# Performance work log

Hardware: AMD Instinct MI355X
Metric: run time of the kernel (lower is better)

Reference implementation:

```python
import jax, jax.numpy as jnp
import numpy as np

INPUT_DIM = 8
HIDDEN_DIM = 128
MID = 50
T = 4096
# original: tsteps = linspace(t0, t1, int(2 + (t1-t0)//0.1)); with t1-t0 == 1.0,
# 1.0//0.1 == 9.0 in float arithmetic -> 11 points -> 10 uniform Euler substeps.
K_SUB = 10


def setup_inputs() -> dict:
    key = jax.random.key(0)
    ks = jax.random.split(key, 12)
    x = jax.random.normal(ks[0], (T, INPUT_DIM), dtype=jnp.float32)
    # arange pairs (2i, 2i+1): every interval has t1 - t0 == 1.0
    dt = jnp.arange(T * 2, dtype=jnp.float32).reshape(T, 2)
    s = 0.1  # init.normal_(std=0.1) in LODEFunc; reuse for heads
    W1 = jax.random.normal(ks[1], (INPUT_DIM + HIDDEN_DIM, MID), dtype=jnp.float32) * s
    b1 = jnp.zeros((MID,), dtype=jnp.float32)
    W2 = jax.random.normal(ks[2], (MID, HIDDEN_DIM), dtype=jnp.float32) * s
    b2 = jnp.zeros((HIDDEN_DIM,), dtype=jnp.float32)
    Wls1 = jax.random.normal(ks[3], (HIDDEN_DIM, HIDDEN_DIM), dtype=jnp.float32) * s
    bls1 = jax.random.normal(ks[4], (HIDDEN_DIM,), dtype=jnp.float32) * s
    wls2 = jax.random.normal(ks[5], (HIDDEN_DIM,), dtype=jnp.float32) * s
    bls2 = jax.random.normal(ks[6], (), dtype=jnp.float32) * s
    Wlm1 = jax.random.normal(ks[7], (HIDDEN_DIM, HIDDEN_DIM), dtype=jnp.float32) * s
    blm1 = jax.random.normal(ks[8], (HIDDEN_DIM,), dtype=jnp.float32) * s
    return {"x": x, "dt": dt, "W1": W1, "b1": b1, "W2": W2, "b2": b2,
            "Wls1": Wls1, "bls1": bls1, "wls2": wls2, "bls2": bls2,
            "Wlm1": Wlm1, "blm1": blm1}


def reference(x, dt, W1, b1, W2, b2, Wls1, bls1, wls2, bls2, Wlm1, blm1):
    def ode_func(z, xi):
        # LODEFunc: tanh(Linear(tanh(Linear(cat(z, x)))))
        zx = jnp.concatenate([z, xi])  # [H + I]
        h1 = jnp.tanh(zx @ W1 + b1)    # [50]
        return jnp.tanh(h1 @ W2 + b2)  # [H]

    def step(z, inp):
        xi, dti = inp
        hstep = (dti[1] - dti[0]) / K_SUB  # uniform Euler step (0 interval -> no-op)
        z = jax.lax.fori_loop(0, K_SUB, lambda j, zz: zz + hstep * ode_func(zz, xi), z)
        pre_sigma = jnp.tanh(z @ Wls1 + bls1)
        sigma = jax.nn.softplus(pre_sigma @ wls2 + bls2)
        pre_mu = jnp.tanh(z @ Wlm1 + blm1)
        mu = pre_mu @ wls2 + bls2  # NOTE: original reuses self.ls2 for mu (faithful)
        return z, (mu, sigma)

    z0 = jnp.zeros((HIDDEN_DIM,), dtype=x.dtype)
    _, (mu_out, sigma_out) = jax.lax.scan(step, z0, (x, dt))
    return mu_out[:, None], sigma_out[:, None]  # each [T, 1]
```

## Files before the change

### kernel.cpp

```cpp
#include <hip/hip_runtime.h>
#include <hip/hip_bf16.h>

#define T_STEPS 4096
#define HID 128
#define INP 8
#define MID 50
#define KSUB 10

typedef float v2f __attribute__((ext_vector_type(2)));

__device__ __forceinline__ v2f mk2(float a, float b){ v2f r; r.x = a; r.y = b; return r; }
__device__ __forceinline__ v2f bc2(float s){ v2f r; r.x = s; r.y = s; return r; }

__device__ __forceinline__ v2f fma2(v2f a, v2f b, v2f c){
#if __has_builtin(__builtin_elementwise_fma)
    return __builtin_elementwise_fma(a, b, c);
#else
    c.x = fmaf(a.x, b.x, c.x); c.y = fmaf(a.y, b.y, c.y); return c;
#endif
}

__device__ __forceinline__ float rlane(float v, int i){
    return __int_as_float(__builtin_amdgcn_readlane(__float_as_int(v), i));
}

__device__ __forceinline__ float fast_tanh(float x){
    float e = __expf(2.0f * x);
    return 1.0f - 2.0f / (e + 1.0f);
}
__device__ __forceinline__ float softplus_f(float x){
    return (x > 20.0f) ? x : __logf(1.0f + __expf(x));
}

__device__ __forceinline__ void wg_barrier(){
    asm volatile("s_waitcnt lgkmcnt(0)\n\ts_barrier" ::: "memory");
}

__global__ __launch_bounds__(384, 2)
void lode_kernel(const float* __restrict__ x, const float* __restrict__ dt,
                 const float* __restrict__ W1, const float* __restrict__ b1,
                 const float* __restrict__ W2, const float* __restrict__ b2,
                 const float* __restrict__ Wls1, const float* __restrict__ bls1,
                 const float* __restrict__ wls2, const float* __restrict__ bls2,
                 const float* __restrict__ Wlm1, const float* __restrict__ blm1,
                 float* __restrict__ out)
{
    __shared__ __align__(16) float pbuf[2][4][64];
    __shared__ __align__(16) float zsnap[2][HID];
    __shared__ __align__(16) float WhL[2][HID*HID];

    const int tid = threadIdx.x;
    const int wid = tid >> 6;
    const int l   = tid & 63;

    {
        float4*       d0 = reinterpret_cast<float4*>(&WhL[0][0]);
        const float4* s0 = reinterpret_cast<const float4*>(Wls1);
        for (int i = tid; i < HID*HID/4; i += 384) d0[i] = s0[i];
        float4*       d1 = reinterpret_cast<float4*>(&WhL[1][0]);
        const float4* s1 = reinterpret_cast<const float4*>(Wlm1);
        for (int i = tid; i < HID*HID/4; i += 384) d1[i] = s1[i];
    }
    wg_barrier();

    if (wid < 4){
        __builtin_amdgcn_s_setprio(1);
        const int base = wid << 5;
        const int lc   = (l < MID) ? l : 0;

        float w1h[32];
        #pragma unroll
        for (int i = 0; i < 32; ++i){
            const float v = W1[(base + i)*MID + lc];
            w1h[i] = (l < MID) ? v : 0.0f;
        }
        float w1x[INP];
        #pragma unroll
        for (int j = 0; j < INP; ++j){
            const float v = W1[(HID + j)*MID + lc];
            w1x[j] = (wid == 0 && l < MID) ? v : 0.0f;
        }
        const float b1c = (wid == 0 && l < MID) ? b1[lc] : 0.0f;

        const int jc = base + (l & 31);
        float w2c[MID];
        #pragma unroll
        for (int k = 0; k < MID; ++k) w2c[k] = W2[k*HID + jc];
        const float b2c = b2[jc];

        float zj = 0.0f;

        float4 xa  = *reinterpret_cast<const float4*>(&x[0]);
        float4 xb  = *reinterpret_cast<const float4*>(&x[4]);
        float2 dtc = *reinterpret_cast<const float2*>(&dt[0]);

        for (int t = 0; t < T_STEPS; ++t){
            const int tn = (t + 1 < T_STEPS) ? t + 1 : t;
            const float4 xan = *reinterpret_cast<const float4*>(&x[tn*INP]);
            const float4 xbn = *reinterpret_cast<const float4*>(&x[tn*INP + 4]);
            const float2 dtn = *reinterpret_cast<const float2*>(&dt[2*tn]);

            float xacc = b1c;
            xacc = fmaf(xa.x, w1x[0], xacc); xacc = fmaf(xa.y, w1x[1], xacc);
            xacc = fmaf(xa.z, w1x[2], xacc); xacc = fmaf(xa.w, w1x[3], xacc);
            xacc = fmaf(xb.x, w1x[4], xacc); xacc = fmaf(xb.y, w1x[5], xacc);
            xacc = fmaf(xb.z, w1x[6], xacc); xacc = fmaf(xb.w, w1x[7], xacc);
            const float hstep = (dtc.y - dtc.x) * (1.0f / KSUB);

            #pragma unroll 2
            for (int s = 0; s < KSUB; ++s){
                float a0 = xacc, a1 = 0.0f, a2 = 0.0f, a3 = 0.0f;
                #pragma unroll
                for (int i = 0; i < 32; i += 4){
                    a0 = fmaf(rlane(zj, i+0), w1h[i+0], a0);
                    a1 = fmaf(rlane(zj, i+1), w1h[i+1], a1);
                    a2 = fmaf(rlane(zj, i+2), w1h[i+2], a2);
                    a3 = fmaf(rlane(zj, i+3), w1h[i+3], a3);
                }
                pbuf[s & 1][wid][l] = (a0 + a1) + (a2 + a3);
                wg_barrier();

                const float p0 = pbuf[s & 1][0][l];
                const float p1 = pbuf[s & 1][1][l];
                const float p2 = pbuf[s & 1][2][l];
                const float p3 = pbuf[s & 1][3][l];
                const float h1v = fast_tanh((p0 + p1) + (p2 + p3));

                float d0 = 0.0f, d1 = 0.0f, d2 = 0.0f, d3 = 0.0f;
                #pragma unroll
                for (int k = 0; k < 48; k += 4){
                    d0 = fmaf(rlane(h1v, k+0), w2c[k+0], d0);
                    d1 = fmaf(rlane(h1v, k+1), w2c[k+1], d1);
                    d2 = fmaf(rlane(h1v, k+2), w2c[k+2], d2);
                    d3 = fmaf(rlane(h1v, k+3), w2c[k+3], d3);
                }
                d0 = fmaf(rlane(h1v, 48), w2c[48], d0);
                d1 = fmaf(rlane(h1v, 49), w2c[49], d1);
                const float d = (d0 + d1) + (d2 + d3);
                zj += hstep * fast_tanh(b2c + d);
            }

            if (l < 32) zsnap[t & 1][base + l] = zj;

            xa = xan; xb = xbn; dtc = dtn;
        }
        wg_barrier();
    } else {
        const float* __restrict__ Wh = (wid == 4) ? &WhL[0][0] : &WhL[1][0];
        const float* __restrict__ bh = (wid == 4) ? bls1 : blm1;
        const v2f bhp   = mk2(bh[2*l], bh[2*l+1]);
        const v2f wls2p = mk2(wls2[2*l], wls2[2*l+1]);
        const float bls2s = bls2[0];

        for (int t = 0; t < T_STEPS; ++t){
            v2f acc2 = bhp;
            float r = 0.0f;
            const float* zs = &zsnap[(t - 1) & 1][0];
            #pragma unroll
            for (int s = 0; s < KSUB; ++s){
                wg_barrier();
                if (t == 0) continue;
                if (s < 8){
                    #pragma unroll
                    for (int kk = 0; kk < 4; ++kk){
                        const int k = 16*s + 4*kk;
                        const float4 zv = *reinterpret_cast<const float4*>(&zs[k]);
                        const v2f w0 = *reinterpret_cast<const v2f*>(&Wh[(k+0)*HID + 2*l]);
                        const v2f w1 = *reinterpret_cast<const v2f*>(&Wh[(k+1)*HID + 2*l]);
                        const v2f w2 = *reinterpret_cast<const v2f*>(&Wh[(k+2)*HID + 2*l]);
                        const v2f w3 = *reinterpret_cast<const v2f*>(&Wh[(k+3)*HID + 2*l]);
                        acc2 = fma2(bc2(zv.x), w0, acc2);
                        acc2 = fma2(bc2(zv.y), w1, acc2);
                        acc2 = fma2(bc2(zv.z), w2, acc2);
                        acc2 = fma2(bc2(zv.w), w3, acc2);
                    }
                } else if (s == 8){
                    const float px = fast_tanh(acc2.x);
                    const float py = fast_tanh(acc2.y);
                    r = px*wls2p.x + py*wls2p.y;
                    #pragma unroll
                    for (int off = 1; off < 64; off <<= 1) r += __shfl_xor(r, off, 64);
                } else {
                    if (l == 0){
                        const int ts = t - 1;
                        if (wid == 4) out[T_STEPS + ts] = softplus_f(r + bls2s);
                        else          out[ts]           = r + bls2s;
                    }
                }
            }
        }
        wg_barrier();

        {
            const int ts = T_STEPS - 1;
            const float* zs = &zsnap[ts & 1][0];
            v2f acc2 = bhp;
            #pragma unroll 4
            for (int k = 0; k < HID; k += 4){
                const float4 zv = *reinterpret_cast<const float4*>(&zs[k]);
                const v2f w0 = *reinterpret_cast<const v2f*>(&Wh[(k+0)*HID + 2*l]);
                const v2f w1 = *reinterpret_cast<const v2f*>(&Wh[(k+1)*HID + 2*l]);
                const v2f w2 = *reinterpret_cast<const v2f*>(&Wh[(k+2)*HID + 2*l]);
                const v2f w3 = *reinterpret_cast<const v2f*>(&Wh[(k+3)*HID + 2*l]);
                acc2 = fma2(bc2(zv.x), w0, acc2);
                acc2 = fma2(bc2(zv.y), w1, acc2);
                acc2 = fma2(bc2(zv.z), w2, acc2);
                acc2 = fma2(bc2(zv.w), w3, acc2);
            }
            const float px = fast_tanh(acc2.x);
            const float py = fast_tanh(acc2.y);
            float r = px*wls2p.x + py*wls2p.y;
            #pragma unroll
            for (int off = 1; off < 64; off <<= 1) r += __shfl_xor(r, off, 64);
            if (l == 0){
                if (wid == 4) out[T_STEPS + ts] = softplus_f(r + bls2s);
                else          out[ts]           = r + bls2s;
            }
        }
    }
}

extern "C" void kernel_launch(void* const* d_in, const int* in_sizes, int n_in,
                              void* d_out, int out_size, void* d_ws, size_t ws_size,
                              hipStream_t stream)
{
    const float* x    = (const float*)d_in[0];
    const float* dt   = (const float*)d_in[1];
    const float* W1   = (const float*)d_in[2];
    const float* b1   = (const float*)d_in[3];
    const float* W2   = (const float*)d_in[4];
    const float* b2   = (const float*)d_in[5];
    const float* Wls1 = (const float*)d_in[6];
    const float* bls1 = (const float*)d_in[7];
    const float* wls2 = (const float*)d_in[8];
    const float* bls2 = (const float*)d_in[9];
    const float* Wlm1 = (const float*)d_in[10];
    const float* blm1 = (const float*)d_in[11];
    float* out = (float*)d_out;

    hipLaunchKernelGGL(lode_kernel, dim3(1), dim3(384), 0, stream,
                       x, dt, W1, b1, W2, b2, Wls1, bls1, wls2, bls2, Wlm1, blm1, out);
}
```

Measured before the change: 18.48 ms.

## Split W2 reduction across lane pairs with packed FMA from LDS

Each lane pair now owns one hidden output and splits the 50-term W2 dot product in half. Each half reads h1 from a per-wave LDS buffer with float4 loads and accumulates with packed two-wide FMAs, then the halves combine through a lane xor shuffle. This replaces 50 serial readlane broadcasts per substep on the serial critical path. The z layout moves to even lanes, so the W1 readlane indices are remapped. It adds an LDS write/read round trip and a cross-lane shuffle inside each substep.

```diff
diff --git a/kernel.cpp b/kernel.cpp
--- a/kernel.cpp
+++ b/kernel.cpp
@@ -47,6 +47,7 @@
 {
     __shared__ __align__(16) float pbuf[2][4][64];
     __shared__ __align__(16) float zsnap[2][HID];
+    __shared__ __align__(16) float h1own[4][64];
     __shared__ __align__(16) float WhL[2][HID*HID];
 
     const int tid = threadIdx.x;
@@ -82,10 +83,17 @@
         }
         const float b1c = (wid == 0 && l < MID) ? b1[lc] : 0.0f;
 
-        const int jc = base + (l & 31);
-        float w2c[MID];
+        const int p  = l & 1;
+        const int jc = base + (l >> 1);
+        const int kb = p ? 28 : 0;
+        v2f w2p[14];
         #pragma unroll
-        for (int k = 0; k < MID; ++k) w2c[k] = W2[k*HID + jc];
+        for (int i = 0; i < 14; ++i){
+            const int k0 = kb + 2*i, k1 = kb + 2*i + 1;
+            const float a = (k0 < MID) ? W2[k0*HID + jc] : 0.0f;
+            const float b = (k1 < MID) ? W2[k1*HID + jc] : 0.0f;
+            w2p[i] = mk2(a, b);
+        }
         const float b2c = b2[jc];
 
         float zj = 0.0f;
@@ -112,10 +120,10 @@
                 float a0 = xacc, a1 = 0.0f, a2 = 0.0f, a3 = 0.0f;
                 #pragma unroll
                 for (int i = 0; i < 32; i += 4){
-                    a0 = fmaf(rlane(zj, i+0), w1h[i+0], a0);
-                    a1 = fmaf(rlane(zj, i+1), w1h[i+1], a1);
-                    a2 = fmaf(rlane(zj, i+2), w1h[i+2], a2);
-                    a3 = fmaf(rlane(zj, i+3), w1h[i+3], a3);
+                    a0 = fmaf(rlane(zj, 2*i+0), w1h[i+0], a0);
+                    a1 = fmaf(rlane(zj, 2*i+2), w1h[i+1], a1);
+                    a2 = fmaf(rlane(zj, 2*i+4), w1h[i+2], a2);
+                    a3 = fmaf(rlane(zj, 2*i+6), w1h[i+3], a3);
                 }
                 pbuf[s & 1][wid][l] = (a0 + a1) + (a2 + a3);
                 wg_barrier();
@@ -126,21 +134,21 @@
                 const float p3 = pbuf[s & 1][3][l];
                 const float h1v = fast_tanh((p0 + p1) + (p2 + p3));
 
-                float d0 = 0.0f, d1 = 0.0f, d2 = 0.0f, d3 = 0.0f;
+                h1own[wid][l] = h1v;
+                v2f D0 = bc2(0.0f), D1 = bc2(0.0f);
                 #pragma unroll
-                for (int k = 0; k < 48; k += 4){
-                    d0 = fmaf(rlane(h1v, k+0), w2c[k+0], d0);
-                    d1 = fmaf(rlane(h1v, k+1), w2c[k+1], d1);
-                    d2 = fmaf(rlane(h1v, k+2), w2c[k+2], d2);
-                    d3 = fmaf(rlane(h1v, k+3), w2c[k+3], d3);
+                for (int q = 0; q < 7; ++q){
+                    const float4 hq = *reinterpret_cast<const float4*>(&h1own[wid][kb + 4*q]);
+                    D0 = fma2(mk2(hq.x, hq.y), w2p[2*q  ], D0);
+                    D1 = fma2(mk2(hq.z, hq.w), w2p[2*q+1], D1);
                 }
-                d0 = fmaf(rlane(h1v, 48), w2c[48], d0);
-                d1 = fmaf(rlane(h1v, 49), w2c[49], d1);
-                const float d = (d0 + d1) + (d2 + d3);
+                const v2f DD = D0 + D1;
+                float d = DD.x + DD.y;
+                d += __shfl_xor(d, 1, 64);
                 zj += hstep * fast_tanh(b2c + d);
             }
 
-            if (l < 32) zsnap[t & 1][base + l] = zj;
+            if (p == 0) zsnap[t & 1][jc] = zj;
 
             xa = xan; xb = xbn; dtc = dtn;
         }
```

New measurement: 18.83 ms. Within noise of the previous version (+1.9%).
